# Optimization experiments

Hardware: AMD Instinct MI355X
Metric: run time of the kernel (lower is better)

The kernel has to match this reference:

```python
import jax, jax.numpy as jnp
import numpy as np

H = 16        # num_heads
D_HEAD = 128  # head_dim
D = H * D_HEAD  # hidden_size = 2048


def setup_inputs() -> dict:
    key = jax.random.key(0)
    ks = jax.random.split(key, 9)
    s = 1.0 / np.sqrt(D)
    x = jax.random.normal(ks[0], (2, 2048, D), dtype=jnp.float32)
    Wq = jax.random.uniform(ks[1], (D, D), jnp.float32, -s, s)
    bq = jax.random.uniform(ks[2], (D,), jnp.float32, -s, s)
    Wk = jax.random.uniform(ks[3], (D, D), jnp.float32, -s, s)
    bk = jax.random.uniform(ks[4], (D,), jnp.float32, -s, s)
    Wv = jax.random.uniform(ks[5], (D, D), jnp.float32, -s, s)
    bv = jax.random.uniform(ks[6], (D,), jnp.float32, -s, s)
    Wo = jax.random.uniform(ks[7], (D, D), jnp.float32, -s, s)
    bo = jax.random.uniform(ks[8], (D,), jnp.float32, -s, s)
    return {"x": x, "Wq": Wq, "bq": bq, "Wk": Wk, "bk": bk,
            "Wv": Wv, "bv": bv, "Wo": Wo, "bo": bo}


def reference(x, Wq, bq, Wk, bk, Wv, bv, Wo, bo):
    B, T, _ = x.shape
    # Linear projections (torch Linear: x @ W.T + b)
    Q = x @ Wq.T + bq
    K = x @ Wk.T + bk
    V = x @ Wv.T + bv
    # [B, T, H, Dh] -> [B, H, T, Dh]
    Q = Q.reshape(B, T, H, D_HEAD).transpose(0, 2, 1, 3)
    K = K.reshape(B, T, H, D_HEAD).transpose(0, 2, 1, 3)
    V = V.reshape(B, T, H, D_HEAD).transpose(0, 2, 1, 3)
    scores = jnp.einsum('bhqd,bhkd->bhqk', Q, K) / jnp.sqrt(jnp.float32(D_HEAD))
    causal = jnp.tril(jnp.ones((T, T), dtype=bool))
    scores = jnp.where(causal, scores, -jnp.inf)
    probs = jax.nn.softmax(scores, axis=-1)
    ctx = jnp.einsum('bhqk,bhkd->bhqd', probs, V)  # [B, H, T, Dh]
    merged = ctx.transpose(0, 2, 1, 3).reshape(B, T, D)
    return merged @ Wo.T + bo
```

## Files before the change

### kernel.cpp

```cpp
#include <hip/hip_runtime.h>
#include <hip/hip_bf16.h>
#include <math.h>

typedef unsigned short ushort_t;
typedef short bf16x8 __attribute__((ext_vector_type(8)));
typedef float f32x4 __attribute__((ext_vector_type(4)));
typedef float f32x16 __attribute__((ext_vector_type(16)));

#define NH 16
#define DH 128
#define DM 2048
#define TSEQ 2048
#define BT 4096

__device__ __forceinline__ void async16(const void* g, void* l) {
  __builtin_amdgcn_global_load_lds(
      (const __attribute__((address_space(1))) void*)g,
      (__attribute__((address_space(3))) void*)l, 16, 0, 0);
}

__device__ __forceinline__ f32x4 mfma16(bf16x8 a, bf16x8 b, f32x4 c) {
  return __builtin_amdgcn_mfma_f32_16x16x32_bf16(a, b, c, 0, 0, 0);
}
__device__ __forceinline__ f32x16 mfma32(bf16x8 a, bf16x8 b, f32x16 c) {
  return __builtin_amdgcn_mfma_f32_32x32x16_bf16(a, b, c, 0, 0, 0);
}

__device__ __forceinline__ ushort_t f2bf(float f) {
  __hip_bfloat16 h = __float2bfloat16(f);
  return *reinterpret_cast<ushort_t*>(&h);
}
__device__ __forceinline__ unsigned cvtpk_bf16(float lo, float hi_) {
  unsigned r;
  asm("v_cvt_pk_bf16_f32 %0, %1, %2" : "=v"(r) : "v"(lo), "v"(hi_));
  return r;
}
__device__ __forceinline__ float fexp2(float x) {
  float r; asm("v_exp_f32 %0, %1" : "=v"(r) : "v"(x)); return r;
}

__global__ void cvt_all_kernel(const float* __restrict__ x,
                               const float* __restrict__ Wq, const float* __restrict__ Wk,
                               const float* __restrict__ Wv, const float* __restrict__ Wo,
                               ushort_t* __restrict__ xb,
                               ushort_t* __restrict__ Wqb, ushort_t* __restrict__ Wkb,
                               ushort_t* __restrict__ Wvb, ushort_t* __restrict__ Wob)
{
  const int i = blockIdx.x * blockDim.x + threadIdx.x;
  const float* src; ushort_t* dst; int off;
  if (i < (1 << 21)) {
    src = x; dst = xb; off = i;
  } else {
    const int j = i - (1 << 21);
    const int w = j >> 20;
    off = j & ((1 << 20) - 1);
    src = (w == 0) ? Wq : (w == 1) ? Wk : (w == 2) ? Wv : Wo;
    dst = (w == 0) ? Wqb : (w == 1) ? Wkb : (w == 2) ? Wvb : Wob;
  }
  const float4 v = reinterpret_cast<const float4*>(src)[off];
  ushort4 u;
  u.x = f2bf(v.x); u.y = f2bf(v.y); u.z = f2bf(v.z); u.w = f2bf(v.w);
  reinterpret_cast<ushort4*>(dst)[off] = u;
}

template<int MODE>
__global__ __launch_bounds__(256)
void gemm_kernel(const ushort_t* __restrict__ A,
                 const ushort_t* __restrict__ W_0, const ushort_t* __restrict__ W_1,
                 const ushort_t* __restrict__ W_2,
                 const float* __restrict__ b_0, const float* __restrict__ b_1,
                 const float* __restrict__ b_2,
                 ushort_t* __restrict__ outQ, ushort_t* __restrict__ outK,
                 ushort_t* __restrict__ outVt, float* __restrict__ outF)
{
  constexpr int K = DM;
  constexpr int NZ = (MODE == 0) ? 3 : 1;
  __shared__ __attribute__((aligned(16))) ushort_t As[128 * 64];
  __shared__ __attribute__((aligned(16))) ushort_t Bs[128 * 64];

  const int F = (int)blockIdx.x + 16 * ((int)blockIdx.y + 32 * (int)blockIdx.z);
  const int xcd = F & 7;
  const int k_ = F >> 3;
  const int m_t = k_ / (2 * NZ);
  const int r_ = k_ % (2 * NZ);
  const int z = r_ % NZ;
  const int b_ = r_ / NZ;
  const int n0 = (xcd * 2 + b_) * 128;
  const int m0 = m_t * 128;

  const ushort_t* Wp = (MODE == 0) ? (z == 0 ? W_0 : (z == 1 ? W_1 : W_2)) : W_0;
  const float* bias  = (MODE == 0) ? (z == 0 ? b_0 : (z == 1 ? b_1 : b_2)) : b_0;

  const int tid = threadIdx.x;
  const int w = tid >> 6, l = tid & 63;
  const int wm = w >> 1, wn = w & 1;
  const int l15 = l & 15, l4 = l >> 4;

  f32x4 zero = {0.f, 0.f, 0.f, 0.f};
  f32x4 acc[4][4];
#pragma unroll
  for (int i = 0; i < 4; ++i)
#pragma unroll
    for (int j = 0; j < 4; ++j) acc[i][j] = zero;

  for (int k0 = 0; k0 < K; k0 += 64) {
    __syncthreads();
#pragma unroll
    for (int i = 0; i < 4; ++i) {
      const int rb = (i * 4 + w) * 8;
      const int r = rb + (l >> 3);
      const int c = ((l & 7) * 8) ^ ((r & 7) * 8);
      async16(A  + (size_t)(m0 + r) * K + k0 + c, &As[rb * 64]);
      async16(Wp + (size_t)(n0 + r) * K + k0 + c, &Bs[rb * 64]);
    }
    __syncthreads();
#pragma unroll
    for (int ks = 0; ks < 2; ++ks) {
      bf16x8 af[4], bfr[4];
#pragma unroll
      for (int mf = 0; mf < 4; ++mf) {
        const int row = wm * 64 + mf * 16 + l15;
        const int byte_ = row * 128 + ((l4 * 16 + ks * 64) ^ ((row & 7) << 4));
        af[mf] = *reinterpret_cast<const bf16x8*>(reinterpret_cast<const char*>(As) + byte_);
      }
#pragma unroll
      for (int nf = 0; nf < 4; ++nf) {
        const int row = wn * 64 + nf * 16 + l15;
        const int byte_ = row * 128 + ((l4 * 16 + ks * 64) ^ ((row & 7) << 4));
        bfr[nf] = *reinterpret_cast<const bf16x8*>(reinterpret_cast<const char*>(Bs) + byte_);
      }
#pragma unroll
      for (int mf = 0; mf < 4; ++mf)
#pragma unroll
        for (int nf = 0; nf < 4; ++nf)
          acc[mf][nf] = mfma16(af[mf], bfr[nf], acc[mf][nf]);
    }
  }

#pragma unroll
  for (int nf = 0; nf < 4; ++nf) {
    const int n = n0 + wn * 64 + nf * 16 + l15;
    const float bv = bias[n];
#pragma unroll
    for (int mf = 0; mf < 4; ++mf) {
#pragma unroll
      for (int r = 0; r < 4; ++r) {
        const int m = m0 + wm * 64 + mf * 16 + l4 * 4 + r;
        const float v = acc[mf][nf][r] + bv;
        if (MODE == 1) {
          outF[(size_t)m * DM + n] = v;
        } else {
          const int b = m >> 11, t = m & 2047;
          const int hh = n >> 7, d = n & 127;
          const ushort_t val = f2bf(v);
          if (z == 2) {
            outVt[((size_t)(b * NH + hh) * DH + d) * TSEQ + t] = val;
          } else {
            ushort_t* dst = (z == 0) ? outQ : outK;
            dst[((size_t)(b * NH + hh) * TSEQ + t) * DH + d] = val;
          }
        }
      }
    }
  }
}

__device__ __forceinline__ void stage_kv(const ushort_t* __restrict__ Kg,
                                         const ushort_t* __restrict__ Vt,
                                         size_t kbase, size_t vbase, int kv0,
                                         ushort_t* KsB, ushort_t* VsB, int tid)
{
#pragma unroll
  for (int i = 0; i < 4; ++i) {
    const int idx = i * 256 + tid;
    const int r = idx >> 4, ch = idx & 15;
    const int c = (ch ^ (r & 7)) * 8;
    async16(Kg + kbase + (size_t)(kv0 + r) * DH + c, KsB + idx * 8);
  }
#pragma unroll
  for (int i = 0; i < 4; ++i) {
    const int idx = i * 256 + tid;
    const int d = idx >> 3, ch = idx & 7;
    const int c = (ch ^ (d & 7)) * 8;
    async16(Vt + vbase + (size_t)d * TSEQ + kv0 + c, VsB + idx * 8);
  }
}

__global__ __launch_bounds__(256)
void attn_kernel(const ushort_t* __restrict__ Q, const ushort_t* __restrict__ Kg,
                 const ushort_t* __restrict__ Vt, ushort_t* __restrict__ ctx)
{
  __shared__ __attribute__((aligned(16))) ushort_t Ks[2][64 * 128];
  __shared__ __attribute__((aligned(16))) ushort_t Vs[2][128 * 64];

  const int fid = (int)blockIdx.x + 16 * (int)blockIdx.y;
  const int xcd = fid & 7;
  const int s   = fid >> 3;
  const int bh  = xcd * 4 + (s & 3);
  const int qt  = (s < 32) ? (15 - (s >> 2)) : ((s - 32) >> 2);

  const int tid = threadIdx.x, w = tid >> 6, l = tid & 63;
  const int l31 = l & 31, hi = l >> 5;
  const size_t kbase = (size_t)bh * TSEQ * DH;
  const size_t vbase = (size_t)bh * DH * TSEQ;
  const int bq0 = qt * 128;
  const int wq0 = bq0 + w * 32;
  const int NT = qt * 2 + 2;
  const int q = wq0 + l31;
  const float C2 = 0.12753842f;
  const float NEG = -3.0e38f;

  bf16x8 aq[8];
  {
    const ushort_t* qp = Q + kbase + (size_t)q * DH + hi * 8;
#pragma unroll
    for (int st = 0; st < 8; ++st)
      aq[st] = *reinterpret_cast<const bf16x8*>(qp + st * 16);
  }

  f32x16 o[4] = {};
  float m_r = NEG, l_r = 0.f;

  stage_kv(Kg, Vt, kbase, vbase, 0, Ks[0], Vs[0], tid);

  for (int kt = 0; kt < NT; ++kt) {
    const int kv0 = kt * 64, cur = kt & 1;
    if (kt + 1 < NT) {
      stage_kv(Kg, Vt, kbase, vbase, kv0 + 64, Ks[cur ^ 1], Vs[cur ^ 1], tid);
      asm volatile("s_waitcnt vmcnt(8)" ::: "memory");
    } else {
      asm volatile("s_waitcnt vmcnt(0)" ::: "memory");
    }
    __builtin_amdgcn_s_barrier();

    if (kv0 <= wq0 + 31) {
      const char* ksb = reinterpret_cast<const char*>(Ks[cur]);
      f32x16 s0 = {}, s1 = {};
      __builtin_amdgcn_s_setprio(1);
#pragma unroll
      for (int st = 0; st < 8; ++st) {
        const int byt = l31 * 256 + ((hi * 16 + st * 32) ^ ((l31 & 7) << 4));
        bf16x8 ak0 = *reinterpret_cast<const bf16x8*>(ksb + byt);
        bf16x8 ak1 = *reinterpret_cast<const bf16x8*>(ksb + byt + 8192);
        s0 = mfma32(ak0, aq[st], s0);
        s1 = mfma32(ak1, aq[st], s1);
      }
      __builtin_amdgcn_s_setprio(0);

      if (kv0 + 63 > wq0) {
#pragma unroll
        for (int r = 0; r < 16; ++r) {
          const int kvl = kv0 + (r & 3) + 8 * (r >> 2) + 4 * hi;
          if (kvl > q)      s0[r] = NEG;
          if (kvl + 32 > q) s1[r] = NEG;
        }
      }

      float t8[8];
#pragma unroll
      for (int r = 0; r < 8; ++r)
        t8[r] = fmaxf(fmaxf(s0[r], s0[r + 8]), fmaxf(s1[r], s1[r + 8]));
#pragma unroll
      for (int r = 0; r < 4; ++r) t8[r] = fmaxf(t8[r], t8[r + 4]);
      float mt = fmaxf(fmaxf(t8[0], t8[1]), fmaxf(t8[2], t8[3]));
      mt = fmaxf(mt, __shfl_xor(mt, 32));

      const float mnew = fmaxf(m_r, mt);
      if (!__all(mt <= m_r + 16.0f)) {
        const float alpha = fexp2((m_r - mnew) * C2);
        l_r *= alpha;
#pragma unroll
        for (int d0 = 0; d0 < 4; ++d0) o[d0] *= alpha;
        m_r = mnew;
      }

#pragma unroll
      for (int r = 0; r < 16; ++r) {
        s0[r] = fexp2((s0[r] - m_r) * C2);
        s1[r] = fexp2((s1[r] - m_r) * C2);
      }
      float sm[8];
#pragma unroll
      for (int r = 0; r < 8; ++r) sm[r] = (s0[r] + s0[r + 8]) + (s1[r] + s1[r + 8]);
#pragma unroll
      for (int r = 0; r < 4; ++r) sm[r] += sm[r + 4];
      float ls = (sm[0] + sm[1]) + (sm[2] + sm[3]);
      ls += __shfl_xor(ls, 32);
      l_r += ls;

      const char* vsb = reinterpret_cast<const char*>(Vs[cur]);
#pragma unroll
      for (int ks = 0; ks < 4; ++ks) {
        float pj[8];
#pragma unroll
        for (int j = 0; j < 8; ++j)
          pj[j] = (ks >> 1) ? s1[(ks & 1) * 8 + j] : s0[(ks & 1) * 8 + j];
        unsigned cA = cvtpk_bf16(pj[0], pj[1]);
        unsigned cB = cvtpk_bf16(pj[2], pj[3]);
        unsigned cC = cvtpk_bf16(pj[4], pj[5]);
        unsigned cD = cvtpk_bf16(pj[6], pj[7]);
        asm volatile("v_permlane32_swap_b32 %0, %1" : "+v"(cA), "+v"(cC));
        asm volatile("v_permlane32_swap_b32 %0, %1" : "+v"(cB), "+v"(cD));
        union { unsigned u[4]; bf16x8 v; } pa;
        pa.u[0] = cA; pa.u[1] = cB; pa.u[2] = cC; pa.u[3] = cD;
        __builtin_amdgcn_s_setprio(1);
#pragma unroll
        for (int d0 = 0; d0 < 4; ++d0) {
          const int byt = (d0 * 32 + l31) * 128 + ((ks * 32 + hi * 16) ^ ((l31 & 7) << 4));
          bf16x8 av = *reinterpret_cast<const bf16x8*>(vsb + byt);
          o[d0] = mfma32(av, pa.v, o[d0]);
        }
        __builtin_amdgcn_s_setprio(0);
      }
    }
    asm volatile("" ::: "memory");
    __builtin_amdgcn_s_barrier();
  }

  const size_t obase = (size_t)(bh >> 4) * TSEQ * DM + (size_t)(bh & 15) * DH;
  const float inv = 1.0f / l_r;
  ushort_t* cp = ctx + obase + (size_t)q * DM + hi * 4;
#pragma unroll
  for (int d0 = 0; d0 < 4; ++d0) {
#pragma unroll
    for (int g = 0; g < 4; ++g) {
      ushort4 u;
      u.x = f2bf(o[d0][4 * g + 0] * inv);
      u.y = f2bf(o[d0][4 * g + 1] * inv);
      u.z = f2bf(o[d0][4 * g + 2] * inv);
      u.w = f2bf(o[d0][4 * g + 3] * inv);
      *reinterpret_cast<ushort4*>(cp + d0 * 32 + 8 * g) = u;
    }
  }
}

extern "C" void kernel_launch(void* const* d_in, const int* in_sizes, int n_in,
                              void* d_out, int out_size, void* d_ws, size_t ws_size,
                              hipStream_t stream) {
  const float* x  = (const float*)d_in[0];
  const float* Wq = (const float*)d_in[1];
  const float* bq = (const float*)d_in[2];
  const float* Wk = (const float*)d_in[3];
  const float* bk = (const float*)d_in[4];
  const float* Wv = (const float*)d_in[5];
  const float* bv = (const float*)d_in[6];
  const float* Wo = (const float*)d_in[7];
  const float* bo = (const float*)d_in[8];
  float* out = (float*)d_out;

  char* ws = (char*)d_ws;
  ushort_t* xb  = (ushort_t*)ws;  ws += (size_t)BT * DM * 2;
  ushort_t* Wqb = (ushort_t*)ws;  ws += (size_t)DM * DM * 2;
  ushort_t* Wkb = (ushort_t*)ws;  ws += (size_t)DM * DM * 2;
  ushort_t* Wvb = (ushort_t*)ws;  ws += (size_t)DM * DM * 2;
  ushort_t* Wob = (ushort_t*)ws;  ws += (size_t)DM * DM * 2;
  ushort_t* Qb  = (ushort_t*)ws;  ws += (size_t)BT * DM * 2;
  ushort_t* Kb  = (ushort_t*)ws;  ws += (size_t)BT * DM * 2;
  ushort_t* Vtb = (ushort_t*)ws;  ws += (size_t)BT * DM * 2;
  ushort_t* ctxb = xb;

  cvt_all_kernel<<<6 * (1 << 20) / 256, 256, 0, stream>>>(
      x, Wq, Wk, Wv, Wo, xb, Wqb, Wkb, Wvb, Wob);

  gemm_kernel<0><<<dim3(16, 32, 3), 256, 0, stream>>>(
      xb, Wqb, Wkb, Wvb, bq, bk, bv, Qb, Kb, Vtb, nullptr);

  attn_kernel<<<dim3(TSEQ / 128, 32), 256, 0, stream>>>(Qb, Kb, Vtb, ctxb);

  gemm_kernel<1><<<dim3(16, 32, 1), 256, 0, stream>>>(
      ctxb, Wob, nullptr, nullptr, bo, nullptr, nullptr,
      nullptr, nullptr, nullptr, out);
}
```

Before: 301.5 us.

## Double-buffer GEMM LDS tiles with async prefetch and raise MFMA priority

The projection GEMM now keeps two LDS buffers per operand. It issues the async global-to-LDS loads for the next K tile before computing the current one, and uses vmcnt waits plus raw barriers in place of two __syncthreads per step. It wraps the MFMA block in s_setprio to favour the math wavefronts. It also drops the XCD-aware block remapping in favour of plain blockIdx tiling. The goal is to hide global load latency behind MFMA work, at the cost of twice the LDS per block, which may lower occupancy, and possibly worse L2 locality without the XCD swizzle.

```diff
diff --git a/kernel.cpp b/kernel.cpp
--- a/kernel.cpp
+++ b/kernel.cpp
@@ -63,6 +63,22 @@
   reinterpret_cast<ushort4*>(dst)[off] = u;
 }
 
+__device__ __forceinline__ void stage_ab(const ushort_t* __restrict__ A,
+                                         const ushort_t* __restrict__ Wp,
+                                         int m0, int n0, int k0,
+                                         ushort_t* AsB, ushort_t* BsB,
+                                         int w, int l)
+{
+#pragma unroll
+  for (int i = 0; i < 4; ++i) {
+    const int rb = (i * 4 + w) * 8;
+    const int r = rb + (l >> 3);
+    const int c = ((l & 7) * 8) ^ ((r & 7) * 8);
+    async16(A  + (size_t)(m0 + r) * DM + k0 + c, AsB + rb * 64);
+    async16(Wp + (size_t)(n0 + r) * DM + k0 + c, BsB + rb * 64);
+  }
+}
+
 template<int MODE>
 __global__ __launch_bounds__(256)
 void gemm_kernel(const ushort_t* __restrict__ A,
@@ -73,24 +89,16 @@
                  ushort_t* __restrict__ outQ, ushort_t* __restrict__ outK,
                  ushort_t* __restrict__ outVt, float* __restrict__ outF)
 {
-  constexpr int K = DM;
-  constexpr int NZ = (MODE == 0) ? 3 : 1;
-  __shared__ __attribute__((aligned(16))) ushort_t As[128 * 64];
-  __shared__ __attribute__((aligned(16))) ushort_t Bs[128 * 64];
-
-  const int F = (int)blockIdx.x + 16 * ((int)blockIdx.y + 32 * (int)blockIdx.z);
-  const int xcd = F & 7;
-  const int k_ = F >> 3;
-  const int m_t = k_ / (2 * NZ);
-  const int r_ = k_ % (2 * NZ);
-  const int z = r_ % NZ;
-  const int b_ = r_ / NZ;
-  const int n0 = (xcd * 2 + b_) * 128;
-  const int m0 = m_t * 128;
-
+  constexpr int NK = DM / 64;
+  __shared__ __attribute__((aligned(16))) ushort_t As[2][128 * 64];
+  __shared__ __attribute__((aligned(16))) ushort_t Bs[2][128 * 64];
+
+  const int z = (MODE == 0) ? blockIdx.z : 0;
   const ushort_t* Wp = (MODE == 0) ? (z == 0 ? W_0 : (z == 1 ? W_1 : W_2)) : W_0;
   const float* bias  = (MODE == 0) ? (z == 0 ? b_0 : (z == 1 ? b_1 : b_2)) : b_0;
 
+  const int n0 = blockIdx.x * 128;
+  const int m0 = blockIdx.y * 128;
   const int tid = threadIdx.x;
   const int w = tid >> 6, l = tid & 63;
   const int wm = w >> 1, wn = w & 1;
@@ -103,17 +111,18 @@
 #pragma unroll
     for (int j = 0; j < 4; ++j) acc[i][j] = zero;
 
-  for (int k0 = 0; k0 < K; k0 += 64) {
-    __syncthreads();
-#pragma unroll
-    for (int i = 0; i < 4; ++i) {
-      const int rb = (i * 4 + w) * 8;
-      const int r = rb + (l >> 3);
-      const int c = ((l & 7) * 8) ^ ((r & 7) * 8);
-      async16(A  + (size_t)(m0 + r) * K + k0 + c, &As[rb * 64]);
-      async16(Wp + (size_t)(n0 + r) * K + k0 + c, &Bs[rb * 64]);
-    }
-    __syncthreads();
+  stage_ab(A, Wp, m0, n0, 0, As[0], Bs[0], w, l);
+
+  for (int kt = 0; kt < NK; ++kt) {
+    const int cur = kt & 1;
+    if (kt + 1 < NK) {
+      stage_ab(A, Wp, m0, n0, (kt + 1) * 64, As[cur ^ 1], Bs[cur ^ 1], w, l);
+      asm volatile("s_waitcnt vmcnt(8)" ::: "memory");
+    } else {
+      asm volatile("s_waitcnt vmcnt(0)" ::: "memory");
+    }
+    __builtin_amdgcn_s_barrier();
+
 #pragma unroll
     for (int ks = 0; ks < 2; ++ks) {
       bf16x8 af[4], bfr[4];
@@ -121,20 +130,24 @@
       for (int mf = 0; mf < 4; ++mf) {
         const int row = wm * 64 + mf * 16 + l15;
         const int byte_ = row * 128 + ((l4 * 16 + ks * 64) ^ ((row & 7) << 4));
-        af[mf] = *reinterpret_cast<const bf16x8*>(reinterpret_cast<const char*>(As) + byte_);
+        af[mf] = *reinterpret_cast<const bf16x8*>(reinterpret_cast<const char*>(As[cur]) + byte_);
       }
 #pragma unroll
       for (int nf = 0; nf < 4; ++nf) {
         const int row = wn * 64 + nf * 16 + l15;
         const int byte_ = row * 128 + ((l4 * 16 + ks * 64) ^ ((row & 7) << 4));
-        bfr[nf] = *reinterpret_cast<const bf16x8*>(reinterpret_cast<const char*>(Bs) + byte_);
-      }
+        bfr[nf] = *reinterpret_cast<const bf16x8*>(reinterpret_cast<const char*>(Bs[cur]) + byte_);
+      }
+      __builtin_amdgcn_s_setprio(1);
 #pragma unroll
       for (int mf = 0; mf < 4; ++mf)
 #pragma unroll
         for (int nf = 0; nf < 4; ++nf)
           acc[mf][nf] = mfma16(af[mf], bfr[nf], acc[mf][nf]);
-    }
+      __builtin_amdgcn_s_setprio(0);
+    }
+    asm volatile("" ::: "memory");
+    __builtin_amdgcn_s_barrier();
   }
 
 #pragma unroll
```

Result: faster. 278.5 us (-7.6%).
